# Kernel optimization log

Measured on AMD Instinct MI355X. Metric: run time of the kernel, lower is better.

The kernel has to match this reference:

```python
import jax, jax.numpy as jnp
import numpy as np

B, D_IN, D_OUT, E, K, RH = 8192, 1024, 1024, 8, 2, 128

def setup_inputs() -> dict:
    key = jax.random.key(0)
    ks = jax.random.split(key, 7)
    s_in = 1.0 / np.sqrt(D_IN)
    s_rh = 1.0 / np.sqrt(RH)
    return {
        "x": jax.random.normal(ks[0], (B, D_IN), jnp.float32),
        # router: Linear(D_IN, RH) -> tanh -> Linear(RH, E) -> softmax
        "rw1": jax.random.uniform(ks[1], (D_IN, RH), jnp.float32, -s_in, s_in),
        "rb1": jax.random.uniform(ks[2], (RH,), jnp.float32, -s_in, s_in),
        "rw2": jax.random.uniform(ks[3], (RH, E), jnp.float32, -s_rh, s_rh),
        "rb2": jax.random.uniform(ks[4], (E,), jnp.float32, -s_rh, s_rh),
        # experts: E x Linear(D_IN, D_OUT)
        "ew": jax.random.uniform(ks[5], (E, D_IN, D_OUT), jnp.float32, -s_in, s_in),
        "eb": jax.random.uniform(ks[6], (E, D_OUT), jnp.float32, -s_in, s_in),
    }

def reference(x, rw1, rb1, rw2, rb2, ew, eb):
    # router (glu_on=False, gim_input=None): softmax over experts (dim=1)
    h = jnp.tanh(x @ rw1 + rb1)                       # [B, RH]
    probs = jax.nn.softmax(h @ rw2 + rb2, axis=1)     # [B, E]
    ws, ib = jax.lax.top_k(probs, K)                  # [B, K] each
    nws = jax.nn.softmax(ws, axis=1)                  # renormalized top-k weights
    # per-expert GEMM on all tokens (dense-equivalent of masked dispatch)
    y = jnp.einsum("bd,edf->bef", x, ew) + eb         # [B, E, D_OUT]
    # combine weights: scatter nws into [B, E] at selected expert slots
    comb = jnp.zeros((x.shape[0], E), x.dtype).at[
        jnp.arange(x.shape[0])[:, None], ib].add(nws)  # [B, E]
    # weighted scatter-combine (output_type='sum')
    return jnp.einsum("be,bef->bf", comb, y)          # [B, D_OUT]
```

## Files before the change

### kernel.cpp

```cpp
#include <hip/hip_runtime.h>

#define B_TOK   8192
#define D_IN    1024
#define D_OUT   1024
#define NEXP    8
#define RH      128
#define MAXTILES 136
#define MAXSLOTS (MAXTILES*128)

typedef __attribute__((ext_vector_type(8))) short v8s;
typedef __attribute__((ext_vector_type(8))) unsigned short v8u;
typedef __attribute__((ext_vector_type(4))) unsigned short v4u;
typedef __attribute__((ext_vector_type(4))) float v4f;

__device__ __forceinline__ unsigned short f2bf(float f){
  unsigned int u = __float_as_uint(f);
  u += 0x7fffu + ((u >> 16) & 1u);
  return (unsigned short)(u >> 16);
}
__device__ __forceinline__ float bf2f(unsigned short s){
  return __uint_as_float(((unsigned int)s) << 16);
}
__device__ __forceinline__ void gload16(const void* g, void* l){
  __builtin_amdgcn_global_load_lds(
      (const __attribute__((address_space(1))) unsigned int*)g,
      (__attribute__((address_space(3))) unsigned int*)l, 16, 0, 0);
}

__global__ __launch_bounds__(256) void k_cvt_ew(const float* __restrict__ ew,
                                                unsigned short* __restrict__ ewT){
  __shared__ float tile[32][33];
  int tx = threadIdx.x, ty = threadIdx.y;
  int n0 = blockIdx.x*32, k0 = blockIdx.y*32, e = blockIdx.z;
  size_t ebase = (size_t)e << 20;
  #pragma unroll
  for (int i=0;i<4;i++){
    int kl = ty*4+i;
    tile[kl][tx] = ew[ebase + (size_t)(k0+kl)*1024 + n0 + tx];
  }
  __syncthreads();
  #pragma unroll
  for (int i=0;i<4;i++){
    int nl = ty*4+i;
    ewT[ebase + (size_t)(n0+nl)*1024 + (k0 + tx)] = f2bf(tile[tx][nl]);
  }
}

__global__ __launch_bounds__(256) void k_router(
    const float* __restrict__ x,  const float* __restrict__ rw1,
    const float* __restrict__ rb1,const float* __restrict__ rw2,
    const float* __restrict__ rb2,
    unsigned short* __restrict__ xbf,
    int2* __restrict__ tok_ids, float2* __restrict__ tok_w)
{
  __shared__ float xs [16*68];
  __shared__ float ws [64*132];
  __shared__ float hs [16*132];
  __shared__ float r2s[RH*NEXP];
  __shared__ float ls [16*NEXP];
  int tid  = threadIdx.x;
  int lane = tid & 63, w = tid >> 6;
  int g    = lane >> 4;
  int j    = lane & 15;
  int rh0  = w*32 + j, rh1 = rh0 + 16;
  int tok0 = blockIdx.x * 16;

  {
    *(float4*)(r2s + tid*4) = *(const float4*)(rw2 + tid*4);
  }
  float acc[4][2];
  #pragma unroll
  for (int i=0;i<4;i++){ acc[i][0]=0.f; acc[i][1]=0.f; }

  for (int slab=0; slab<16; ++slab){
    int k0 = slab*64;
    {
      int t = tid >> 4, c4 = tid & 15;
      float4 v = *(const float4*)(x + (size_t)(tok0+t)*D_IN + k0 + c4*4);
      *(float4*)(xs + t*68 + c4*4) = v;
      v4u ub = { f2bf(v.x), f2bf(v.y), f2bf(v.z), f2bf(v.w) };
      *(v4u*)(xbf + (size_t)(tok0+t)*D_IN + k0 + c4*4) = ub;
    }
    #pragma unroll
    for (int i=0;i<8;i++){
      int idx = tid + 256*i;
      int r = idx >> 5, c4 = (idx & 31)*4;
      *(float4*)(ws + r*132 + c4) = *(const float4*)(rw1 + (size_t)(k0+r)*RH + c4);
    }
    __syncthreads();
    #pragma unroll 4
    for (int k=0;k<64;k+=4){
      v4f xv[4];
      #pragma unroll
      for (int i=0;i<4;i++) xv[i] = *(v4f*)(xs + (g*4+i)*68 + k);
      #pragma unroll
      for (int kk=0;kk<4;kk++){
        float w0 = ws[(k+kk)*132 + rh0];
        float w1 = ws[(k+kk)*132 + rh1];
        #pragma unroll
        for (int i=0;i<4;i++){
          acc[i][0] += xv[i][kk] * w0;
          acc[i][1] += xv[i][kk] * w1;
        }
      }
    }
    __syncthreads();
  }
  {
    float b0 = rb1[rh0], b1 = rb1[rh1];
    #pragma unroll
    for (int i=0;i<4;i++){
      hs[(g*4+i)*132 + rh0] = tanhf(acc[i][0] + b0);
      hs[(g*4+i)*132 + rh1] = tanhf(acc[i][1] + b1);
    }
  }
  __syncthreads();
  if (tid < 16*NEXP){
    int t = tid >> 3, e = tid & 7;
    float l = rb2[e];
    #pragma unroll 4
    for (int r=0;r<RH;r++) l += hs[t*132 + r] * r2s[r*8 + e];
    ls[t*8 + e] = l;
  }
  __syncthreads();
  if (tid < 16){
    int t = tid;
    float l[NEXP];
    #pragma unroll
    for (int e=0;e<NEXP;e++) l[e] = ls[t*8 + e];
    float mx = l[0];
    #pragma unroll
    for (int e=1;e<NEXP;e++) mx = fmaxf(mx, l[e]);
    float p[NEXP], s = 0.f;
    #pragma unroll
    for (int e=0;e<NEXP;e++){ p[e] = expf(l[e]-mx); s += p[e]; }
    float inv = 1.f/s;
    #pragma unroll
    for (int e=0;e<NEXP;e++) p[e] *= inv;
    int bi = 0; float bv = p[0]; int si = -1; float sv = -1.f;
    #pragma unroll
    for (int e=1;e<NEXP;e++){
      if (p[e] > bv){ sv = bv; si = bi; bv = p[e]; bi = e; }
      else if (p[e] > sv){ sv = p[e]; si = e; }
    }
    float e1 = expf(sv - bv);
    float n0 = 1.f/(1.f + e1);
    float n1 = 1.f - n0;
    tok_ids[tok0 + t] = make_int2(bi, si);
    tok_w [tok0 + t] = make_float2(n0, n1);
  }
}

__global__ __launch_bounds__(1024) void k_dispatch(
    const int2* __restrict__ tok_ids, const float2* __restrict__ tok_w,
    int* __restrict__ atok, float* __restrict__ aw,
    int* __restrict__ slotA, int* __restrict__ slotB,
    int2* __restrict__ ttab, int* __restrict__ ntiles)
{
  __shared__ int cnt[NEXP], base[NEXP], cur[NEXP];
  __shared__ int tot;
  int tid = threadIdx.x;
  if (tid < NEXP){ cnt[tid]=0; cur[tid]=0; }
  __syncthreads();
  for (int t=tid; t<B_TOK; t+=1024){
    int2 e = tok_ids[t];
    atomicAdd(&cnt[e.x],1);
    atomicAdd(&cnt[e.y],1);
  }
  __syncthreads();
  if (tid==0){
    int b=0, tt=0;
    for (int e=0;e<NEXP;e++){
      base[e]=b;
      int nt = (cnt[e]+127)>>7;
      for (int i=0;i<nt;i++) ttab[tt++] = make_int2(e, b + i*128);
      b += nt*128;
    }
    tot = b; *ntiles = tt;
  }
  __syncthreads();
  int tt_ = tot;
  for (int s=tid; s<tt_; s+=1024){ atok[s]=0; aw[s]=0.f; }
  __syncthreads();
  for (int t=tid; t<B_TOK; t+=1024){
    int2 e = tok_ids[t]; float2 w = tok_w[t];
    int sA = base[e.x] + atomicAdd(&cur[e.x],1);
    atok[sA]=t; aw[sA]=w.x; slotA[t]=sA;
    int sB = base[e.y] + atomicAdd(&cur[e.y],1);
    atok[sB]=t; aw[sB]=w.y; slotB[t]=sB;
  }
}

__global__ __launch_bounds__(256) void k_gemm(
    const unsigned short* __restrict__ xbf, const unsigned short* __restrict__ ewT,
    const float* __restrict__ eb,
    const int* __restrict__ atok, const float* __restrict__ aw,
    const int2* __restrict__ ttab, const int* __restrict__ ntiles,
    unsigned short* __restrict__ Y)
{
  if ((int)blockIdx.x >= *ntiles) return;
  __shared__ __align__(16) unsigned short As[128*64];
  __shared__ __align__(16) unsigned short Bs[128*64];
  __shared__ int   tokS[128];
  __shared__ float wS[128];
  int tid = threadIdx.x;
  int lane = tid & 63, wid = tid >> 6;
  int2 tt = ttab[blockIdx.x];
  int e = tt.x, slot0 = tt.y;
  int ncol0 = blockIdx.y * 128;
  if (tid < 128){ tokS[tid] = atok[slot0 + tid]; wS[tid] = aw[slot0 + tid]; }
  __syncthreads();
  int rsub = wid*8 + (lane >> 3);
  int cbyte = (lane & 7) * 16;
  const char* xB    = (const char*)xbf;
  const char* eBase = (const char*)ewT + ((size_t)e << 21);
  const char* srcA[4]; const char* srcB[4];
  #pragma unroll
  for (int i=0;i<4;i++){
    srcA[i] = xB    + ((size_t)tokS[i*32 + rsub] << 11) + cbyte;
    srcB[i] = eBase + ((size_t)(ncol0 + i*32 + rsub) << 11) + cbyte;
  }
  v4f zero = {0.f,0.f,0.f,0.f};
  v4f acc[4][4];
  #pragma unroll
  for (int mi=0;mi<4;mi++)
    #pragma unroll
    for (int ni=0;ni<4;ni++) acc[mi][ni] = zero;
  int wr = wid >> 1, wc = wid & 1;
  int fr = lane & 15, fq = lane >> 4;
  unsigned Abase = (unsigned)((wr*64 + fr)*64 + fq*8);
  unsigned Bbase = (unsigned)((wc*64 + fr)*64 + fq*8);

  for (int kt=0; kt<16; ++kt){
    int koff = kt*128;
    #pragma unroll
    for (int i=0;i<4;i++)
      gload16(srcA[i] + koff, (char*)As + (i*32 + wid*8)*128);
    #pragma unroll
    for (int i=0;i<4;i++)
      gload16(srcB[i] + koff, (char*)Bs + (i*32 + wid*8)*128);
    __syncthreads();
    #pragma unroll
    for (int kk=0;kk<2;kk++){
      v8s a[4], b[4];
      #pragma unroll
      for (int mi=0;mi<4;mi++) a[mi] = *(const v8s*)(As + Abase + mi*16*64 + kk*32);
      #pragma unroll
      for (int ni=0;ni<4;ni++) b[ni] = *(const v8s*)(Bs + Bbase + ni*16*64 + kk*32);
      #pragma unroll
      for (int mi=0;mi<4;mi++)
        #pragma unroll
        for (int ni=0;ni<4;ni++)
          acc[mi][ni] = __builtin_amdgcn_mfma_f32_16x16x32_bf16(a[mi], b[ni], acc[mi][ni], 0, 0, 0);
    }
    __syncthreads();
  }
  #pragma unroll
  for (int ni=0;ni<4;ni++){
    int cg = ncol0 + wc*64 + ni*16 + fr;
    float ebv = eb[e*D_OUT + cg];
    #pragma unroll
    for (int mi=0;mi<4;mi++){
      int rb0 = wr*64 + mi*16 + fq*4;
      #pragma unroll
      for (int q=0;q<4;q++){
        int r = rb0 + q;
        float v = wS[r] * (acc[mi][ni][q] + ebv);
        Y[(size_t)(slot0 + r)*D_OUT + cg] = f2bf(v);
      }
    }
  }
}

__global__ __launch_bounds__(256) void k_combine(
    const unsigned short* __restrict__ Y,
    const int* __restrict__ slotA, const int* __restrict__ slotB,
    float* __restrict__ out)
{
  int gid = blockIdx.x*256 + threadIdx.x;
  int t = gid >> 7;
  int c = (gid & 127) << 3;
  v8u a = *(const v8u*)(Y + (size_t)slotA[t]*D_OUT + c);
  v8u b = *(const v8u*)(Y + (size_t)slotB[t]*D_OUT + c);
  float4 o0, o1;
  o0.x = bf2f(a[0]) + bf2f(b[0]);
  o0.y = bf2f(a[1]) + bf2f(b[1]);
  o0.z = bf2f(a[2]) + bf2f(b[2]);
  o0.w = bf2f(a[3]) + bf2f(b[3]);
  o1.x = bf2f(a[4]) + bf2f(b[4]);
  o1.y = bf2f(a[5]) + bf2f(b[5]);
  o1.z = bf2f(a[6]) + bf2f(b[6]);
  o1.w = bf2f(a[7]) + bf2f(b[7]);
  *(float4*)(out + (size_t)t*D_OUT + c)     = o0;
  *(float4*)(out + (size_t)t*D_OUT + c + 4) = o1;
}

extern "C" void kernel_launch(void* const* d_in, const int* in_sizes, int n_in,
                              void* d_out, int out_size, void* d_ws, size_t ws_size,
                              hipStream_t stream)
{
  const float* x   = (const float*)d_in[0];
  const float* rw1 = (const float*)d_in[1];
  const float* rb1 = (const float*)d_in[2];
  const float* rw2 = (const float*)d_in[3];
  const float* rb2 = (const float*)d_in[4];
  const float* ew  = (const float*)d_in[5];
  const float* eb  = (const float*)d_in[6];
  float* out = (float*)d_out;

  char* ws = (char*)d_ws;
  size_t o = 0;
  auto alloc = [&](size_t bytes)->char*{
    char* p = ws + o; o = (o + bytes + 255) & ~(size_t)255; return p;
  };
  unsigned short* xbf = (unsigned short*)alloc((size_t)B_TOK*D_IN*2);
  unsigned short* ewT = (unsigned short*)alloc((size_t)NEXP*D_IN*D_OUT*2);
  unsigned short* Y   = (unsigned short*)alloc((size_t)MAXSLOTS*D_OUT*2);
  int2*   tok_ids = (int2*)  alloc(B_TOK*sizeof(int2));
  float2* tok_w   = (float2*)alloc(B_TOK*sizeof(float2));
  int*    atok    = (int*)   alloc(MAXSLOTS*4);
  float*  aw      = (float*) alloc(MAXSLOTS*4);
  int*    slotA   = (int*)   alloc(B_TOK*4);
  int*    slotB   = (int*)   alloc(B_TOK*4);
  int2*   ttab    = (int2*)  alloc(256*sizeof(int2));
  int*    ntil    = (int*)   alloc(256);
  if (o > ws_size) return;

  k_cvt_ew <<<dim3(32,32,NEXP),  dim3(32,8),  0, stream>>>(ew, ewT);
  k_router <<<dim3(512),         dim3(256),   0, stream>>>(x, rw1, rb1, rw2, rb2, xbf, tok_ids, tok_w);
  k_dispatch<<<dim3(1),          dim3(1024),  0, stream>>>(tok_ids, tok_w, atok, aw, slotA, slotB, ttab, ntil);
  k_gemm   <<<dim3(MAXTILES,8),  dim3(256),   0, stream>>>(xbf, ewT, eb, atok, aw, ttab, ntil, Y);
  k_combine<<<dim3(4096),        dim3(256),   0, stream>>>(Y, slotA, slotB, out);
}
```

Measured before the change: 282.7 us.

## Double-buffer LDS, XOR-swizzle tiles, and remap GEMM blocks per XCD

```diff
diff --git a/kernel.cpp b/kernel.cpp
--- a/kernel.cpp
+++ b/kernel.cpp
@@ -198,20 +198,23 @@
     const int2* __restrict__ ttab, const int* __restrict__ ntiles,
     unsigned short* __restrict__ Y)
 {
-  if ((int)blockIdx.x >= *ntiles) return;
-  __shared__ __align__(16) unsigned short As[128*64];
-  __shared__ __align__(16) unsigned short Bs[128*64];
+  int bid = blockIdx.x;
+  int logical = (bid & 7)*MAXTILES + (bid >> 3);
+  int tile = logical >> 3, nb = logical & 7;
+  if (tile >= *ntiles) return;
+  __shared__ __align__(16) unsigned short As[2][128*64];
+  __shared__ __align__(16) unsigned short Bs[2][128*64];
   __shared__ int   tokS[128];
   __shared__ float wS[128];
   int tid = threadIdx.x;
   int lane = tid & 63, wid = tid >> 6;
-  int2 tt = ttab[blockIdx.x];
+  int2 tt = ttab[tile];
   int e = tt.x, slot0 = tt.y;
-  int ncol0 = blockIdx.y * 128;
+  int ncol0 = nb * 128;
   if (tid < 128){ tokS[tid] = atok[slot0 + tid]; wS[tid] = aw[slot0 + tid]; }
   __syncthreads();
   int rsub = wid*8 + (lane >> 3);
-  int cbyte = (lane & 7) * 16;
+  int cbyte = ((lane & 7) ^ (lane >> 3)) * 16;
   const char* xB    = (const char*)xbf;
   const char* eBase = (const char*)ewT + ((size_t)e << 21);
   const char* srcA[4]; const char* srcB[4];
@@ -228,25 +231,47 @@
     for (int ni=0;ni<4;ni++) acc[mi][ni] = zero;
   int wr = wid >> 1, wc = wid & 1;
   int fr = lane & 15, fq = lane >> 4;
-  unsigned Abase = (unsigned)((wr*64 + fr)*64 + fq*8);
-  unsigned Bbase = (unsigned)((wc*64 + fr)*64 + fq*8);
+  int r7 = fr & 7;
+  unsigned c0 = (unsigned)((fq       ^ r7) * 8);
+  unsigned c1 = (unsigned)(((fq + 4) ^ r7) * 8);
+  unsigned ArowBase = (unsigned)((wr*64 + fr)*64);
+  unsigned BrowBase = (unsigned)((wc*64 + fr)*64);
+
+  #pragma unroll
+  for (int i=0;i<4;i++) gload16(srcA[i],       (char*)As[0] + (i*32 + wid*8)*128);
+  #pragma unroll
+  for (int i=0;i<4;i++) gload16(srcB[i],       (char*)Bs[0] + (i*32 + wid*8)*128);
+  __syncthreads();
 
   for (int kt=0; kt<16; ++kt){
-    int koff = kt*128;
-    #pragma unroll
-    for (int i=0;i<4;i++)
-      gload16(srcA[i] + koff, (char*)As + (i*32 + wid*8)*128);
-    #pragma unroll
-    for (int i=0;i<4;i++)
-      gload16(srcB[i] + koff, (char*)Bs + (i*32 + wid*8)*128);
-    __syncthreads();
-    #pragma unroll
-    for (int kk=0;kk<2;kk++){
+    int cur = kt & 1;
+    if (kt < 15){
+      int koff = (kt+1)*128;
+      #pragma unroll
+      for (int i=0;i<4;i++) gload16(srcA[i] + koff, (char*)As[cur^1] + (i*32 + wid*8)*128);
+      #pragma unroll
+      for (int i=0;i<4;i++) gload16(srcB[i] + koff, (char*)Bs[cur^1] + (i*32 + wid*8)*128);
+    }
+    const unsigned short* Ab = As[cur];
+    const unsigned short* Bb = Bs[cur];
+    {
       v8s a[4], b[4];
       #pragma unroll
-      for (int mi=0;mi<4;mi++) a[mi] = *(const v8s*)(As + Abase + mi*16*64 + kk*32);
-      #pragma unroll
-      for (int ni=0;ni<4;ni++) b[ni] = *(const v8s*)(Bs + Bbase + ni*16*64 + kk*32);
+      for (int mi=0;mi<4;mi++) a[mi] = *(const v8s*)(Ab + ArowBase + mi*1024 + c0);
+      #pragma unroll
+      for (int ni=0;ni<4;ni++) b[ni] = *(const v8s*)(Bb + BrowBase + ni*1024 + c0);
+      #pragma unroll
+      for (int mi=0;mi<4;mi++)
+        #pragma unroll
+        for (int ni=0;ni<4;ni++)
+          acc[mi][ni] = __builtin_amdgcn_mfma_f32_16x16x32_bf16(a[mi], b[ni], acc[mi][ni], 0, 0, 0);
+    }
+    {
+      v8s a[4], b[4];
+      #pragma unroll
+      for (int mi=0;mi<4;mi++) a[mi] = *(const v8s*)(Ab + ArowBase + mi*1024 + c1);
+      #pragma unroll
+      for (int ni=0;ni<4;ni++) b[ni] = *(const v8s*)(Bb + BrowBase + ni*1024 + c1);
       #pragma unroll
       for (int mi=0;mi<4;mi++)
         #pragma unroll
@@ -329,6 +354,6 @@
   k_cvt_ew <<<dim3(32,32,NEXP),  dim3(32,8),  0, stream>>>(ew, ewT);
   k_router <<<dim3(512),         dim3(256),   0, stream>>>(x, rw1, rb1, rw2, rb2, xbf, tok_ids, tok_w);
   k_dispatch<<<dim3(1),          dim3(1024),  0, stream>>>(tok_ids, tok_w, atok, aw, slotA, slotB, ttab, ntil);
-  k_gemm   <<<dim3(MAXTILES,8),  dim3(256),   0, stream>>>(xbf, ewT, eb, atok, aw, ttab, ntil, Y);
+  k_gemm   <<<dim3(MAXTILES*8),  dim3(256),   0, stream>>>(xbf, ewT, eb, atok, aw, ttab, ntil, Y);
   k_combine<<<dim3(4096),        dim3(256),   0, stream>>>(Y, slotA, slotB, out);
 }
```

New measurement: 280.4 us. No clear change (-0.8%).
